# Kernel optimization log

Hardware: AMD Instinct MI355X
Metric: run time of the kernel (lower is better)

## Reference

```python
import jax, jax.numpy as jnp
import numpy as np

DIM = 1024
MLP_DIM = 4096
EPS = 1e-5


def layer_norm(x, gamma, beta):
    mean = jnp.mean(x, axis=-1, keepdims=True)
    var = jnp.mean(jnp.square(x - mean), axis=-1, keepdims=True)  # unbiased=False
    return gamma * (x - mean) / jnp.sqrt(var + EPS) + beta


def setup_inputs() -> dict:
    key = jax.random.key(0)
    ks = jax.random.split(key, 12)
    s = 0.02
    return {
        "x": jax.random.normal(ks[0], (4, 2048, DIM), dtype=jnp.float32),
        "gamma1": jnp.ones((DIM,), jnp.float32),
        "beta1": jnp.zeros((DIM,), jnp.float32),
        "gamma2": jnp.ones((DIM,), jnp.float32),
        "beta2": jnp.zeros((DIM,), jnp.float32),
        "Wq": jax.random.normal(ks[1], (DIM, DIM), jnp.float32) * s,
        "bq": jnp.zeros((DIM,), jnp.float32),
        "Wk": jax.random.normal(ks[2], (DIM, DIM), jnp.float32) * s,
        "bk": jnp.zeros((DIM,), jnp.float32),
        "Wv": jax.random.normal(ks[3], (DIM, DIM), jnp.float32) * s,
        "bv": jnp.zeros((DIM,), jnp.float32),
        "W1": jax.random.normal(ks[4], (DIM, MLP_DIM), jnp.float32) * s,
        "b1": jnp.zeros((MLP_DIM,), jnp.float32),
        "W2": jax.random.normal(ks[5], (MLP_DIM, DIM), jnp.float32) * s,
        "b2": jnp.zeros((DIM,), jnp.float32),
    }


def reference(x, gamma1, beta1, gamma2, beta2, Wq, bq, Wk, bk, Wv, bv, W1, b1, W2, b2):
    # Pre-LN attention sub-block (single-head manual attention over full dim)
    residual = x
    h = layer_norm(x, gamma1, beta1)
    q = h @ Wq + bq  # [B,S,D]
    k = h @ Wk + bk
    v = h @ Wv + bv
    scale = 1.0 / jnp.sqrt(jnp.asarray(q.shape[-1], q.dtype))
    scores = jnp.einsum("bsd,btd->bst", q, k) * scale  # [B,S,S]
    attn = jax.nn.softmax(scores, axis=-1)
    x = jnp.einsum("bst,btd->bsd", attn, v) + residual
    # Pre-LN MLP sub-block
    residual = x
    h = layer_norm(x, gamma2, beta2)
    h = jax.nn.gelu(h @ W1 + b1, approximate=False)  # torch F.gelu exact
    x = h @ W2 + b2 + residual
    return x
```

## Files before the change

kernel.cpp:

```cpp
#include <hip/hip_runtime.h>
#include <hip/hip_bf16.h>
#include <math.h>

typedef __bf16 bf16x8 __attribute__((ext_vector_type(8)));
typedef float  f32x4  __attribute__((ext_vector_type(4)));
typedef __hip_bfloat16 bf16;

#define DIM  1024
#define MLPD 4096
#define NB   4
#define SEQ  2048
#define ROWS (NB * SEQ)

__device__ __forceinline__ void gload_lds16(const void* g, void* l) {
  __builtin_amdgcn_global_load_lds(
      (__attribute__((address_space(1))) void*)(g),
      (__attribute__((address_space(3))) void*)(l), 16, 0, 0);
}

__device__ __forceinline__ void bar() {
  asm volatile("" ::: "memory");
  __builtin_amdgcn_s_barrier();
  asm volatile("" ::: "memory");
}

template <int N>
__device__ __forceinline__ void vmw() {
  asm volatile("s_waitcnt vmcnt(%0)" ::"n"(N) : "memory");
}

__device__ __forceinline__ float gelu_exact_fast(float v) {
  const float x  = v * 0.70710678118654752f;
  const float ax = fabsf(x);
  const float t  = __builtin_amdgcn_rcpf(1.0f + 0.3275911f * ax);
  const float p  = t * (0.254829592f +
                   t * (-0.284496736f +
                   t * (1.421413741f +
                   t * (-1.453152027f + t * 1.061405429f))));
  float erf = 1.0f - p * __expf(-x * x);
  erf = copysignf(erf, x);
  return 0.5f * v * (1.0f + erf);
}

template <int EPI>
__global__ __launch_bounds__(512, 2) void gemm256(
    const bf16* __restrict__ A,  long aBatch, int lda,
    const bf16* __restrict__ Bt, long bBatch, int ldb,
    void* __restrict__ Cout,     long cBatch, int ldc,
    const float* __restrict__ bias, int K, float scale)
{
  extern __shared__ char smem[];

  const int gx = gridDim.x, gy = gridDim.y;
  int flat = blockIdx.x + gx * (blockIdx.y + gy * blockIdx.z);
  const int nwg = gx * gy * gridDim.z;
  flat = (flat & 7) * (nwg >> 3) + (flat >> 3);
  const int bx = flat % gx;
  const int t2 = flat / gx;
  const int by = t2 % gy;
  const int bz = t2 / gy;

  const long rowBase = (long)by * 256;
  const long colBase = (long)bx * 256;
  const long ldaB = (long)lda * 2, ldbB = (long)ldb * 2;
  const char* Ag = (const char*)(A + bz * aBatch + rowBase * lda);
  const char* Bg = (const char*)(Bt + bz * bBatch + colBase * ldb);

  const int tid  = threadIdx.x;
  const int lane = tid & 63;
  const int wave = tid >> 6;
  const int wm = wave >> 2, wn = wave & 3;
  const int fr = lane & 15, fq = lane >> 4;
  const int fh2 = fr >> 1;
  const int sA = (((fr & 1) << 2) | fq) ^ fh2;
  const int rdCom = fh2 * 128 + sA * 16;

  long offA[2], offB[2];
#pragma unroll
  for (int li = 0; li < 2; ++li) {
    const int d = li * 512 + tid;
    {
      const int wms = d >> 9, kks = (d >> 8) & 1, w = d & 255;
      const int pr = w >> 3, s = w & 7, u = s ^ (pr & 7);
      offA[li] = (long)(wms * 128 + pr * 2 + (u >> 2)) * ldaB +
                 kks * 64 + (u & 3) * 16;
    }
    {
      const int wns = d >> 8, kkb = (d >> 7) & 1, w = d & 127;
      const int pr = w >> 3, s = w & 7, u = s ^ (pr & 7);
      offB[li] = (long)(wns * 64 + pr * 2 + (u >> 2)) * ldbB +
                 kkb * 64 + (u & 3) * 16;
    }
  }
  const int dstOff = tid * 16;
  const long aHalf = ldaB << 6;
  const long bHalf = ldbB << 5;

  const int NT = K >> 6;

  bf16x8 a[4][2], b[2][2][2];
  f32x4 acc[8][4] = {};

#define STG_A(J, mh)                                                           \
  do {                                                                         \
    char* _d = smem + (((J) & 1) << 16) + (mh) * 16384 + dstOff;               \
    const char* _s = Ag + (J) * 128 + (mh) * aHalf;                            \
    gload_lds16(_s + offA[0], _d);                                             \
    gload_lds16(_s + offA[1], _d + 8192);                                      \
  } while (0)

#define STG_B(J, nh)                                                           \
  do {                                                                         \
    char* _d = smem + (((J) & 1) << 16) + 32768 + (nh) * 16384 + dstOff;       \
    const char* _s = Bg + (J) * 128 + (nh) * bHalf;                            \
    gload_lds16(_s + offB[0], _d);                                             \
    gload_lds16(_s + offB[1], _d + 8192);                                      \
  } while (0)

#define LDA(mh, J)                                                             \
  do {                                                                         \
    const char* _b = smem + (((J) & 1) << 16) + (mh) * 16384 + wm * 8192 +     \
                     rdCom;                                                    \
    _Pragma("unroll") for (int m = 0; m < 4; ++m)                              \
      _Pragma("unroll") for (int kk = 0; kk < 2; ++kk)                         \
        a[m][kk] = *(const bf16x8*)(_b + kk * 4096 + m * 1024);                \
  } while (0)

#define LDB(nh, J)                                                             \
  do {                                                                         \
    const char* _b = smem + (((J) & 1) << 16) + 32768 + (nh) * 16384 +         \
                     wn * 4096 + rdCom;                                        \
    _Pragma("unroll") for (int n = 0; n < 2; ++n)                              \
      _Pragma("unroll") for (int kk = 0; kk < 2; ++kk)                         \
        b[nh][n][kk] = *(const bf16x8*)(_b + kk * 2048 + n * 1024);            \
  } while (0)

#define MM(mh, nh)                                                             \
  do {                                                                         \
    __builtin_amdgcn_s_setprio(1);                                             \
    _Pragma("unroll") for (int m = 0; m < 4; ++m)                              \
      _Pragma("unroll") for (int n = 0; n < 2; ++n)                            \
        _Pragma("unroll") for (int kk = 0; kk < 2; ++kk)                       \
          acc[(mh) * 4 + m][(nh) * 2 + n] =                                    \
              __builtin_amdgcn_mfma_f32_16x16x32_bf16(                         \
                  a[m][kk], b[nh][n][kk], acc[(mh) * 4 + m][(nh) * 2 + n],     \
                  0, 0, 0);                                                    \
    __builtin_amdgcn_s_setprio(0);                                             \
  } while (0)

#define LGKM0 asm volatile("s_waitcnt lgkmcnt(0)" ::: "memory")

#define TILE(J, S1, S2, VN)                                                    \
  do {                                                                         \
    LDA(0, J); LDB(0, J);                                                      \
    if (S1) STG_A((J) + 1, 1);                                                 \
    bar(); LGKM0; MM(0, 0); bar();                                             \
    LDB(1, J);                                                                 \
    if (S2) STG_A((J) + 2, 0);                                                 \
    bar(); LGKM0; MM(0, 1); bar();                                             \
    LDA(1, J);                                                                 \
    if (S2) STG_B((J) + 2, 0);                                                 \
    bar(); LGKM0; MM(1, 1); bar();                                             \
    if (S2) STG_B((J) + 2, 1);                                                 \
    vmw<VN>(); bar(); MM(1, 0); bar();                                         \
  } while (0)

  STG_A(0, 0); STG_B(0, 0); STG_B(0, 1); STG_A(0, 1);
  STG_A(1, 0); STG_B(1, 0); STG_B(1, 1);
  vmw<6>(); bar();

  for (int j = 0; j < NT - 2; ++j) TILE(j, true, true, 6);
  TILE(NT - 2, true, false, 0);
  TILE(NT - 1, false, false, 63);

#undef STG_A
#undef STG_B
#undef LDA
#undef LDB
#undef MM
#undef TILE

#pragma unroll
  for (int mh = 0; mh < 2; ++mh)
#pragma unroll
    for (int m = 0; m < 4; ++m)
#pragma unroll
      for (int nh = 0; nh < 2; ++nh)
#pragma unroll
        for (int n = 0; n < 2; ++n) {
          const long col = colBase + wn * 64 + nh * 32 + n * 16 + fr;
#pragma unroll
          for (int e = 0; e < 4; ++e) {
            const long r = rowBase + wm * 128 + mh * 64 + m * 16 + fq * 4 + e;
            float v = acc[mh * 4 + m][nh * 2 + n][e];
            if constexpr (EPI == 0) {
              v += bias[col];
              ((bf16*)Cout)[bz * cBatch + r * ldc + col] = __float2bfloat16(v);
            } else {
              ((bf16*)Cout)[bz * cBatch + r * ldc + col] =
                  __float2bfloat16(v * scale);
            }
          }
        }
}

template <int EPI>
__global__ __launch_bounds__(256, 4) void gemm128(
    const bf16* __restrict__ A,  long aBatch, int lda,
    const bf16* __restrict__ Bt, long bBatch, int ldb,
    void* __restrict__ Cout,     long cBatch, int ldc,
    const float* __restrict__ bias,
    const float* __restrict__ resid, long rBatch, int ldr,
    int K, float scale)
{
  __shared__ char smem[2][16384];

  const int gx = gridDim.x, gy = gridDim.y;
  const int n = gx * gy * gridDim.z;
  const int f = blockIdx.x + gx * (blockIdx.y + gy * blockIdx.z);
  const int o = (f & 7) * (n >> 3) + (f >> 3);
  const int sx = gx >> 3;
  int st = o >> 6;
  const int w = o & 63;
  const int spz = sx * (gy >> 3);
  const int bz = st / spz; st -= bz * spz;
  const int sty = st / sx, stx = st - sty * sx;
  const int by = sty * 8 + (w >> 3), bx = stx * 8 + (w & 7);

  const long rowBase = (long)by * 128;
  const long colBase = (long)bx * 128;
  const long ldaB = (long)lda * 2, ldbB = (long)ldb * 2;
  const char* Ag = (const char*)(A + bz * aBatch + rowBase * lda);
  const char* Bg = (const char*)(Bt + bz * bBatch + colBase * ldb);

  const int tid  = threadIdx.x;
  const int lane = tid & 63;
  const int wave = tid >> 6;
  const int wm = wave >> 1, wn = wave & 1;
  const int fr = lane & 15, fq = lane >> 4;

  const int fh = fr >> 1;
  const int sA = (((fr & 1) << 2) | fq) ^ fh;
  const int laneRd = fh * 128 + sA * 16;
  const int abase = wm * 4096 + laneRd;
  const int bbase = 8192 + wn * 4096 + laneRd;

  const int t0   = wave * 128 + lane;
  const int r2   = t0 >> 3;
  const int u0   = (t0 & 7) ^ (r2 & 7);
  const int row0 = r2 * 2 + (u0 >> 2);
  const int kc0  = u0 & 3;
  const char* aSrc0 = Ag + (long)row0 * ldaB + kc0 * 16;
  const char* aSrc1 = aSrc0 + 16 * ldaB;
  const char* bSrc0 = Bg + (long)row0 * ldbB + kc0 * 16;
  const char* bSrc1 = bSrc0 + 16 * ldbB;
  const int doff = wave * 2048 + lane * 16;

  const int NT = K >> 5;
  f32x4 acc[4][4] = {};

#define STAGE(WB)                                                              \
  do {                                                                         \
    gload_lds16(aSrc0, &smem[WB][doff]);                                       \
    gload_lds16(aSrc1, &smem[WB][doff + 1024]);                                \
    gload_lds16(bSrc0, &smem[WB][8192 + doff]);                                \
    gload_lds16(bSrc1, &smem[WB][8192 + doff + 1024]);                         \
    aSrc0 += 64; aSrc1 += 64; bSrc0 += 64; bSrc1 += 64;                        \
  } while (0)

#define READMM(RB)                                                             \
  do {                                                                         \
    const char* _r = &smem[RB][0];                                             \
    bf16x8 av[4], bv_[4];                                                      \
    _Pragma("unroll") for (int m = 0; m < 4; ++m)                              \
      av[m] = *(const bf16x8*)(_r + abase + m * 1024);                         \
    _Pragma("unroll") for (int nn = 0; nn < 4; ++nn)                           \
      bv_[nn] = *(const bf16x8*)(_r + bbase + nn * 1024);                      \
    __builtin_amdgcn_s_setprio(1);                                             \
    _Pragma("unroll") for (int m = 0; m < 4; ++m)                              \
      _Pragma("unroll") for (int nn = 0; nn < 4; ++nn)                         \
        acc[m][nn] = __builtin_amdgcn_mfma_f32_16x16x32_bf16(                  \
            av[m], bv_[nn], acc[m][nn], 0, 0, 0);                              \
    __builtin_amdgcn_s_setprio(0);                                             \
  } while (0)

  for (int t = 0; t < NT; t += 2) {
    STAGE(0);
    STAGE(1);
    vmw<0>(); bar();
    READMM(0);
    READMM(1);
    bar();
  }

#undef STAGE
#undef READMM

#pragma unroll
  for (int m = 0; m < 4; ++m) {
#pragma unroll
    for (int nn = 0; nn < 4; ++nn) {
      const long col = colBase + wn * 64 + nn * 16 + fr;
#pragma unroll
      for (int e = 0; e < 4; ++e) {
        const long r = rowBase + wm * 64 + m * 16 + fq * 4 + e;
        float v = acc[m][nn][e];
        if constexpr (EPI == 2) {
          v += resid[bz * rBatch + r * ldr + col];
          ((float*)Cout)[bz * cBatch + r * ldc + col] = v;
        } else if constexpr (EPI == 3) {
          v += bias[col];
          ((bf16*)Cout)[bz * cBatch + r * ldc + col] =
              __float2bfloat16(gelu_exact_fast(v));
        } else if constexpr (EPI == 4) {
          v += bias[col] + resid[r * (long)ldr + col];
          ((float*)Cout)[bz * cBatch + r * ldc + col] = v;
        } else {
          v += bias[r];
          ((bf16*)Cout)[bz * cBatch + r * ldc + col] = __float2bfloat16(v);
        }
      }
    }
  }
}

__global__ __launch_bounds__(256) void ln_kernel(
    const float* __restrict__ x, const float* __restrict__ gamma,
    const float* __restrict__ beta, bf16* __restrict__ out)
{
  const long row = blockIdx.x;
  const float4 v = ((const float4*)(x + row * DIM))[threadIdx.x];
  float s  = v.x + v.y + v.z + v.w;
  float ss = v.x * v.x + v.y * v.y + v.z * v.z + v.w * v.w;
  const int lane = threadIdx.x & 63, wave = threadIdx.x >> 6;
#pragma unroll
  for (int o = 32; o; o >>= 1) { s += __shfl_xor(s, o); ss += __shfl_xor(ss, o); }
  __shared__ float rs[4], rss[4];
  if (lane == 0) { rs[wave] = s; rss[wave] = ss; }
  __syncthreads();
  s  = rs[0] + rs[1] + rs[2] + rs[3];
  ss = rss[0] + rss[1] + rss[2] + rss[3];
  const float mean = s * (1.0f / DIM);
  const float var  = ss * (1.0f / DIM) - mean * mean;
  const float rstd = rsqrtf(var + 1e-5f);
  const float4 g = ((const float4*)gamma)[threadIdx.x];
  const float4 b = ((const float4*)beta)[threadIdx.x];
  union { bf16 h[4]; uint2 u; } pk;
  pk.h[0] = __float2bfloat16(g.x * (v.x - mean) * rstd + b.x);
  pk.h[1] = __float2bfloat16(g.y * (v.y - mean) * rstd + b.y);
  pk.h[2] = __float2bfloat16(g.z * (v.z - mean) * rstd + b.z);
  pk.h[3] = __float2bfloat16(g.w * (v.w - mean) * rstd + b.w);
  ((uint2*)(out + row * DIM))[threadIdx.x] = pk.u;
}

__global__ __launch_bounds__(256) void softmax_kernel(bf16* __restrict__ scores)
{
  const long row = blockIdx.x;
  bf16* rp = scores + row * (long)SEQ;
  union { bf16 h[8]; uint4 u; } in;
  in.u = ((const uint4*)rp)[threadIdx.x];
  float f[8];
#pragma unroll
  for (int j = 0; j < 8; ++j) f[j] = __bfloat162float(in.h[j]);
  const int lane = threadIdx.x & 63, wave = threadIdx.x >> 6;
  float mx = f[0];
#pragma unroll
  for (int j = 1; j < 8; ++j) mx = fmaxf(mx, f[j]);
#pragma unroll
  for (int o = 32; o; o >>= 1) mx = fmaxf(mx, __shfl_xor(mx, o));
  __shared__ float rm[4], rsum[4];
  if (lane == 0) rm[wave] = mx;
  __syncthreads();
  mx = fmaxf(fmaxf(rm[0], rm[1]), fmaxf(rm[2], rm[3]));
  float sum = 0.0f;
#pragma unroll
  for (int j = 0; j < 8; ++j) { f[j] = expf(f[j] - mx); sum += f[j]; }
#pragma unroll
  for (int o = 32; o; o >>= 1) sum += __shfl_xor(sum, o);
  if (lane == 0) rsum[wave] = sum;
  __syncthreads();
  sum = rsum[0] + rsum[1] + rsum[2] + rsum[3];
  const float inv = 1.0f / sum;
  union { bf16 h[8]; uint4 u; } pk;
#pragma unroll
  for (int j = 0; j < 8; ++j) pk.h[j] = __float2bfloat16(f[j] * inv);
  ((uint4*)rp)[threadIdx.x] = pk.u;
}

__global__ __launch_bounds__(256) void prep_kernel(
    const float* __restrict__ Wq, const float* __restrict__ Wk,
    const float* __restrict__ Wv, const float* __restrict__ W1,
    const float* __restrict__ W2,
    const float* __restrict__ bq, const float* __restrict__ bk,
    const float* __restrict__ x, const float* __restrict__ g1,
    const float* __restrict__ be1,
    bf16* __restrict__ WqkT, bf16* __restrict__ WvT,
    bf16* __restrict__ W1T, bf16* __restrict__ W2T,
    float* __restrict__ bqk, bf16* __restrict__ hOut)
{
  int l = blockIdx.x;
  if (l >= 11268) {
    const long row = l - 11268;
    const float4 v = ((const float4*)(x + row * DIM))[threadIdx.x];
    float s  = v.x + v.y + v.z + v.w;
    float ss = v.x * v.x + v.y * v.y + v.z * v.z + v.w * v.w;
    const int lane = threadIdx.x & 63, wave = threadIdx.x >> 6;
#pragma unroll
    for (int o = 32; o; o >>= 1) { s += __shfl_xor(s, o); ss += __shfl_xor(ss, o); }
    __shared__ float rs[4], rss[4];
    if (lane == 0) { rs[wave] = s; rss[wave] = ss; }
    __syncthreads();
    s  = rs[0] + rs[1] + rs[2] + rs[3];
    ss = rss[0] + rss[1] + rss[2] + rss[3];
    const float mean = s * (1.0f / DIM);
    const float var  = ss * (1.0f / DIM) - mean * mean;
    const float rstd = rsqrtf(var + 1e-5f);
    const float4 g = ((const float4*)g1)[threadIdx.x];
    const float4 b = ((const float4*)be1)[threadIdx.x];
    union { bf16 h[4]; uint2 u; } pk;
    pk.h[0] = __float2bfloat16(g.x * (v.x - mean) * rstd + b.x);
    pk.h[1] = __float2bfloat16(g.y * (v.y - mean) * rstd + b.y);
    pk.h[2] = __float2bfloat16(g.z * (v.z - mean) * rstd + b.z);
    pk.h[3] = __float2bfloat16(g.w * (v.w - mean) * rstd + b.w);
    ((uint2*)(hOut + row * DIM))[threadIdx.x] = pk.u;
    return;
  }
  if (l >= 11264) {
    const int i = (l - 11264) * 256 + threadIdx.x;
    bqk[i] = bq[i]; bqk[DIM + i] = bk[i];
    return;
  }
  __shared__ bf16 tile[32][33];
  const float* in; bf16* out; int ldIn, ldOut, gxw;
  if (l < 2048) {
    const int wsel = l >> 10;
    in = wsel ? Wk : Wq;
    out = WqkT + (long)wsel * DIM * DIM;
    l &= 1023; ldIn = DIM; ldOut = DIM; gxw = 32;
  } else if (l < 3072) {
    in = Wv; out = WvT; l -= 2048; ldIn = DIM; ldOut = DIM; gxw = 32;
  } else if (l < 7168) {
    in = W1; out = W1T; l -= 3072; ldIn = MLPD; ldOut = DIM; gxw = 128;
  } else {
    in = W2; out = W2T; l -= 7168; ldIn = DIM; ldOut = MLPD; gxw = 32;
  }
  const int bxx = l % gxw, byy = l / gxw;
  const int c0 = bxx * 32, r0 = byy * 32;
  const int tx = threadIdx.x & 31, ty = threadIdx.x >> 5;
#pragma unroll
  for (int i = 0; i < 32; i += 8)
    tile[ty + i][tx] = __float2bfloat16(in[(long)(r0 + ty + i) * ldIn + c0 + tx]);
  __syncthreads();
#pragma unroll
  for (int i = 0; i < 32; i += 8)
    out[(long)(c0 + ty + i) * ldOut + r0 + tx] = tile[tx][ty + i];
}

extern "C" void kernel_launch(void* const* d_in, const int* in_sizes, int n_in,
                              void* d_out, int out_size, void* d_ws, size_t ws_size,
                              hipStream_t stream) {
  const float* x   = (const float*)d_in[0];
  const float* g1  = (const float*)d_in[1];
  const float* be1 = (const float*)d_in[2];
  const float* g2  = (const float*)d_in[3];
  const float* be2 = (const float*)d_in[4];
  const float* Wq  = (const float*)d_in[5];
  const float* bq  = (const float*)d_in[6];
  const float* Wk  = (const float*)d_in[7];
  const float* bk  = (const float*)d_in[8];
  const float* Wv  = (const float*)d_in[9];
  const float* bv  = (const float*)d_in[10];
  const float* W1  = (const float*)d_in[11];
  const float* b1  = (const float*)d_in[12];
  const float* W2  = (const float*)d_in[13];
  const float* b2  = (const float*)d_in[14];
  float* out = (float*)d_out;

  char* ws = (char*)d_ws;
  bf16* WqkT  = (bf16*)(ws + 0);
  bf16* WvT   = (bf16*)(ws + (4l << 20));
  bf16* W1T   = (bf16*)(ws + (6l << 20));
  bf16* W2T   = (bf16*)(ws + (14l << 20));
  float* bqk  = (float*)(ws + (22l << 20));
  bf16* h     = (bf16*)(ws + (23l << 20));
  bf16* qk    = (bf16*)(ws + (39l << 20));
  bf16* vT    = (bf16*)(ws + (71l << 20));
  bf16* sc    = (bf16*)(ws + (87l << 20));
  bf16* g_act = (bf16*)sc;

  const int SMEM = 131072;
  hipFuncSetAttribute(reinterpret_cast<const void*>(&gemm256<0>),
                      hipFuncAttributeMaxDynamicSharedMemorySize, SMEM);
  hipFuncSetAttribute(reinterpret_cast<const void*>(&gemm256<5>),
                      hipFuncAttributeMaxDynamicSharedMemorySize, SMEM);

  const dim3 blk(256), gblk(512);

  prep_kernel<<<11268 + ROWS, blk, 0, stream>>>(
      Wq, Wk, Wv, W1, W2, bq, bk, x, g1, be1,
      WqkT, WvT, W1T, W2T, bqk, h);

  gemm256<0><<<dim3(8, 32, 1), gblk, SMEM, stream>>>(
      h, 0, DIM, WqkT, 0, DIM, qk, 0, 2 * DIM, bqk, DIM, 1.0f);

  gemm128<6><<<dim3(16, 8, NB), blk, 0, stream>>>(
      WvT, 0, DIM, h, (long)SEQ * DIM, DIM,
      vT, (long)DIM * SEQ, SEQ, bv, nullptr, 0, 0, DIM, 1.0f);

  gemm256<5><<<dim3(8, 8, NB), gblk, SMEM, stream>>>(
      qk, (long)SEQ * 2 * DIM, 2 * DIM, qk + DIM, (long)SEQ * 2 * DIM,
      2 * DIM, sc, (long)SEQ * SEQ, SEQ, nullptr, DIM, 0.03125f);

  softmax_kernel<<<ROWS, blk, 0, stream>>>(sc);

  gemm128<2><<<dim3(8, 16, NB), blk, 0, stream>>>(
      sc, (long)SEQ * SEQ, SEQ, vT, (long)DIM * SEQ, SEQ,
      out, (long)SEQ * DIM, DIM, nullptr, x, (long)SEQ * DIM, DIM, SEQ, 1.0f);

  ln_kernel<<<ROWS, blk, 0, stream>>>(out, g2, be2, h);

  gemm128<3><<<dim3(32, 64, 1), blk, 0, stream>>>(
      h, 0, DIM, W1T, 0, DIM, g_act, 0, MLPD, b1, nullptr, 0, 0, DIM, 1.0f);

  gemm128<4><<<dim3(8, 64, 1), blk, 0, stream>>>(
      g_act, 0, MLPD, W2T, 0, MLPD, out, 0, DIM, b2, out, 0, DIM, MLPD, 1.0f);
}
```

Before: 348.3 us.

## Add four-stage double-pair pipelined GEMM kernel with swizzled block order for MLP

Introduces gemm128d, a 128x128 tile GEMM with four LDS buffers that stages two K-slices ahead while computing on two, and remaps block indices into 8x8 super-tiles spread across XCDs for better L2 reuse. The MLP up- and down-projections now use it. The aim is to hide global-load latency and reduce barrier count per K step. In exchange it uses 64KB of LDS per block, which may limit occupancy, and the index remapping assumes grid dimensions divisible by 8.

Measured after the change: 345.4 us. No clear change (-0.8%).

```diff
diff --git a/kernel.cpp b/kernel.cpp
--- a/kernel.cpp
+++ b/kernel.cpp
@@ -308,16 +308,128 @@
         if constexpr (EPI == 2) {
           v += resid[bz * rBatch + r * ldr + col];
           ((float*)Cout)[bz * cBatch + r * ldc + col] = v;
-        } else if constexpr (EPI == 3) {
+        } else {
+          v += bias[r];
+          ((bf16*)Cout)[bz * cBatch + r * ldc + col] = __float2bfloat16(v);
+        }
+      }
+    }
+  }
+}
+
+template <int EPI>
+__global__ __launch_bounds__(256, 2) void gemm128d(
+    const bf16* __restrict__ A,  long aBatch, int lda,
+    const bf16* __restrict__ Bt, long bBatch, int ldb,
+    void* __restrict__ Cout,     long cBatch, int ldc,
+    const float* __restrict__ bias,
+    const float* __restrict__ resid, long rBatch, int ldr,
+    int K, float scale)
+{
+  __shared__ char smem[4][16384];
+
+  const int gx = gridDim.x, gy = gridDim.y;
+  const int n = gx * gy * gridDim.z;
+  const int f = blockIdx.x + gx * (blockIdx.y + gy * blockIdx.z);
+  const int o = (f & 7) * (n >> 3) + (f >> 3);
+  const int sx = gx >> 3;
+  int st = o >> 6;
+  const int w = o & 63;
+  const int spz = sx * (gy >> 3);
+  const int bz = st / spz; st -= bz * spz;
+  const int sty = st / sx, stx = st - sty * sx;
+  const int by = sty * 8 + (w >> 3), bx = stx * 8 + (w & 7);
+
+  const long rowBase = (long)by * 128;
+  const long colBase = (long)bx * 128;
+  const long ldaB = (long)lda * 2, ldbB = (long)ldb * 2;
+  const char* Ag = (const char*)(A + bz * aBatch + rowBase * lda);
+  const char* Bg = (const char*)(Bt + bz * bBatch + colBase * ldb);
+
+  const int tid  = threadIdx.x;
+  const int lane = tid & 63;
+  const int wave = tid >> 6;
+  const int wm = wave >> 1, wn = wave & 1;
+  const int fr = lane & 15, fq = lane >> 4;
+
+  const int fh = fr >> 1;
+  const int sA = (((fr & 1) << 2) | fq) ^ fh;
+  const int laneRd = fh * 128 + sA * 16;
+  const int abase = wm * 4096 + laneRd;
+  const int bbase = 8192 + wn * 4096 + laneRd;
+
+  const int t0   = wave * 128 + lane;
+  const int r2   = t0 >> 3;
+  const int u0   = (t0 & 7) ^ (r2 & 7);
+  const int row0 = r2 * 2 + (u0 >> 2);
+  const int kc0  = u0 & 3;
+  const char* aSrc0 = Ag + (long)row0 * ldaB + kc0 * 16;
+  const char* aSrc1 = aSrc0 + 16 * ldaB;
+  const char* bSrc0 = Bg + (long)row0 * ldbB + kc0 * 16;
+  const char* bSrc1 = bSrc0 + 16 * ldbB;
+  const int doff = wave * 2048 + lane * 16;
+
+  const int NP = K >> 6;
+  f32x4 acc[4][4] = {};
+
+#define STAGE(WB)                                                              \
+  do {                                                                         \
+    gload_lds16(aSrc0, &smem[WB][doff]);                                       \
+    gload_lds16(aSrc1, &smem[WB][doff + 1024]);                                \
+    gload_lds16(bSrc0, &smem[WB][8192 + doff]);                                \
+    gload_lds16(bSrc1, &smem[WB][8192 + doff + 1024]);                         \
+    aSrc0 += 64; aSrc1 += 64; bSrc0 += 64; bSrc1 += 64;                        \
+  } while (0)
+
+#define READMM(RB)                                                             \
+  do {                                                                         \
+    const char* _r = &smem[RB][0];                                             \
+    bf16x8 av[4], bv_[4];                                                      \
+    _Pragma("unroll") for (int m = 0; m < 4; ++m)                              \
+      av[m] = *(const bf16x8*)(_r + abase + m * 1024);                         \
+    _Pragma("unroll") for (int nn = 0; nn < 4; ++nn)                           \
+      bv_[nn] = *(const bf16x8*)(_r + bbase + nn * 1024);                      \
+    __builtin_amdgcn_s_setprio(1);                                             \
+    _Pragma("unroll") for (int m = 0; m < 4; ++m)                              \
+      _Pragma("unroll") for (int nn = 0; nn < 4; ++nn)                         \
+        acc[m][nn] = __builtin_amdgcn_mfma_f32_16x16x32_bf16(                  \
+            av[m], bv_[nn], acc[m][nn], 0, 0, 0);                              \
+    __builtin_amdgcn_s_setprio(0);                                             \
+  } while (0)
+
+  STAGE(0); STAGE(1);
+
+  for (int it = 0; it < NP; it += 2) {
+    STAGE(2); STAGE(3);
+    vmw<8>(); bar();
+    READMM(0); READMM(1);
+    bar();
+    if (it + 2 < NP) { STAGE(0); STAGE(1); vmw<8>(); }
+    else vmw<0>();
+    bar();
+    READMM(2); READMM(3);
+    bar();
+  }
+
+#undef STAGE
+#undef READMM
+
+#pragma unroll
+  for (int m = 0; m < 4; ++m) {
+#pragma unroll
+    for (int nn = 0; nn < 4; ++nn) {
+      const long col = colBase + wn * 64 + nn * 16 + fr;
+#pragma unroll
+      for (int e = 0; e < 4; ++e) {
+        const long r = rowBase + wm * 64 + m * 16 + fq * 4 + e;
+        float v = acc[m][nn][e];
+        if constexpr (EPI == 3) {
           v += bias[col];
           ((bf16*)Cout)[bz * cBatch + r * ldc + col] =
               __float2bfloat16(gelu_exact_fast(v));
-        } else if constexpr (EPI == 4) {
+        } else {
           v += bias[col] + resid[r * (long)ldr + col];
           ((float*)Cout)[bz * cBatch + r * ldc + col] = v;
-        } else {
-          v += bias[r];
-          ((bf16*)Cout)[bz * cBatch + r * ldc + col] = __float2bfloat16(v);
         }
       }
     }
@@ -519,9 +631,9 @@
 
   ln_kernel<<<ROWS, blk, 0, stream>>>(out, g2, be2, h);
 
-  gemm128<3><<<dim3(32, 64, 1), blk, 0, stream>>>(
+  gemm128d<3><<<dim3(32, 64, 1), blk, 0, stream>>>(
       h, 0, DIM, W1T, 0, DIM, g_act, 0, MLPD, b1, nullptr, 0, 0, DIM, 1.0f);
 
-  gemm128<4><<<dim3(8, 64, 1), blk, 0, stream>>>(
+  gemm128d<4><<<dim3(8, 64, 1), blk, 0, stream>>>(
       g_act, 0, MLPD, W2T, 0, MLPD, out, 0, DIM, b2, out, 0, DIM, MLPD, 1.0f);
 }
```
